# Performance work log

Measured on AMD Instinct MI355X. Metric: run time of the kernel, lower is better.

The kernel has to match this reference:

```python
import jax, jax.numpy as jnp
import numpy as np

POOL = 7                     # cfg.POOLING_SIZE
PRE = 2 * POOL               # pre_pool_size (max_pool=True path)
LEVEL_HW = (256, 128, 64, 32)  # square H=W of P2..P5 for a 1024x1024 image


def setup_inputs() -> dict:
    key = jax.random.key(0)
    ks = jax.random.split(key, 8)
    C = 256
    feats = {f"p{i + 2}": jax.random.normal(ks[i], (1, C, s, s), dtype=jnp.float32)
             for i, s in enumerate(LEVEL_HW)}
    N = 1000
    IMG = 1024.0
    x1 = jax.random.uniform(ks[4], (N,), minval=0.0, maxval=IMG - 33.0)
    y1 = jax.random.uniform(ks[5], (N,), minval=0.0, maxval=IMG - 33.0)
    w = jax.random.uniform(ks[6], (N,), minval=32.0, maxval=512.0)
    h = jax.random.uniform(ks[7], (N,), minval=32.0, maxval=512.0)
    x2 = jnp.minimum(x1 + w, IMG - 1.0)
    y2 = jnp.minimum(y1 + h, IMG - 1.0)
    rois = jnp.stack([jnp.zeros((N,), jnp.float32), x1, y1, x2, y2], axis=1)
    inp = dict(feats)
    inp["rois"] = rois
    return inp


def _crop_pool_fpn(p2, p3, p4, p5, rois):
    """Faithful vectorized version of Network._crop_pool_layer_fpn (max_pool=True).

    Per-ROI FPN level select, affine-grid + bilinear grid_sample
    (align_corners=True semantics, zeros padding), then 2x2 max pool.
    """
    levels = (p2, p3, p4, p5)
    C = p2.shape[1]
    Hm = p2.shape[2]  # largest (P2) map; all levels padded up to this
    # Pad every level into one [L, Hm, Wm, C] array (NHWC for clean gathers).
    feats = jnp.stack([
        jnp.pad(jnp.transpose(f[0], (1, 2, 0)),
                ((0, Hm - f.shape[2]), (0, Hm - f.shape[3]), (0, 0)))
        for f in levels])

    x1, y1, x2, y2 = rois[:, 1], rois[:, 2], rois[:, 3], rois[:, 4]
    w = jnp.where(x2 - x1 <= 0, 1e-14, x2 - x1)
    h = jnp.where(y2 - y1 <= 0, 1e-14, y2 - y1)
    kf = 4.0 + jnp.log2(jnp.sqrt(w * h) / 224.0)   # k0 + log2(sqrt(wh)/224)
    kf = jnp.clip(kf, 2.0, 5.0)                     # clamp BEFORE round (as in source)
    k = jnp.round(kf)
    scale = 2.0 ** k
    lvl = k.astype(jnp.int32) - 2                   # [N] in [0,4)
    x1s, y1s, x2s, y2s = x1 / scale, y1 / scale, x2 / scale, y2 / scale

    # affine_grid(theta) + align_corners=True grid_sample collapses to direct
    # pixel coords: px = (x1+x2)/2 + t*(x2-x1)/2, t = linspace(-1, 1, PRE).
    t = jnp.linspace(-1.0, 1.0, PRE)
    px = (x1s + x2s)[:, None] * 0.5 + t[None, :] * ((x2s - x1s)[:, None] * 0.5)  # [N,PRE]
    py = (y1s + y2s)[:, None] * 0.5 + t[None, :] * ((y2s - y1s)[:, None] * 0.5)
    PX = jnp.broadcast_to(px[:, None, :], (px.shape[0], PRE, PRE))  # [N,PRE,PRE]
    PY = jnp.broadcast_to(py[:, :, None], (py.shape[0], PRE, PRE))

    HWl = jnp.asarray(LEVEL_HW, jnp.float32)[lvl][:, None, None]  # per-ROI level size (square)
    x0 = jnp.floor(PX)
    y0 = jnp.floor(PY)
    dx = PX - x0
    dy = PY - y0

    def gather(yi, xi):
        inb = ((xi >= 0) & (xi < HWl) & (yi >= 0) & (yi < HWl)).astype(feats.dtype)
        yc = jnp.clip(yi, 0, Hm - 1).astype(jnp.int32)
        xc = jnp.clip(xi, 0, Hm - 1).astype(jnp.int32)
        v = feats[lvl[:, None, None], yc, xc]      # [N,PRE,PRE,C]
        return v * inb[..., None]                   # zeros padding

    out = (gather(y0, x0) * ((1 - dy) * (1 - dx))[..., None]
           + gather(y0, x0 + 1) * ((1 - dy) * dx)[..., None]
           + gather(y0 + 1, x0) * (dy * (1 - dx))[..., None]
           + gather(y0 + 1, x0 + 1) * (dy * dx)[..., None])  # [N,PRE,PRE,C]

    crops = jnp.transpose(out, (0, 3, 1, 2))        # [N,C,PRE,PRE]
    N = crops.shape[0]
    crops = crops.reshape(N, C, POOL, 2, POOL, 2).max(axis=(3, 5))  # 2x2 max pool
    return crops                                     # [N,C,POOL,POOL]


def reference(p2, p3, p4, p5, rois):
    return _crop_pool_fpn(p2, p3, p4, p5, rois)
```

## Files before the change

kernel.cpp:

```cpp
#include <hip/hip_runtime.h>
#include <math.h>

#define C_CH 256
#define PRE 14
#define NPOOL 7
#define PIX (NPOOL * NPOOL)
#define OUT_PER_ROI (C_CH * PIX)
#define QTR_OUT (64 * PIX)
#define SROW 68

#define OFF_P2 0
#define OFF_P3 16777216u
#define OFF_P4 20971520u
#define OFF_P5 22020096u
#define WS_ELEMS 22282240u

#define RB 528

static __device__ __forceinline__ unsigned short f2bf(float f) {
    unsigned int u = __float_as_uint(f);
    unsigned int r = (u + 0x7FFFu + ((u >> 16) & 1u)) >> 16;
    return (unsigned short)r;
}
static __device__ __forceinline__ float bfLO(unsigned int u) { return __uint_as_float(u << 16); }
static __device__ __forceinline__ float bfHI(unsigned int u) { return __uint_as_float(u & 0xFFFF0000u); }

static __device__ __forceinline__ float4 bilerp4(uint2 a00, uint2 a01, uint2 a10, uint2 a11, float4 w) {
    float4 r;
    r.x = fmaf(bfLO(a00.x), w.x, fmaf(bfLO(a01.x), w.y, fmaf(bfLO(a10.x), w.z, bfLO(a11.x) * w.w)));
    r.y = fmaf(bfHI(a00.x), w.x, fmaf(bfHI(a01.x), w.y, fmaf(bfHI(a10.x), w.z, bfHI(a11.x) * w.w)));
    r.z = fmaf(bfLO(a00.y), w.x, fmaf(bfLO(a01.y), w.y, fmaf(bfLO(a10.y), w.z, bfLO(a11.y) * w.w)));
    r.w = fmaf(bfHI(a00.y), w.x, fmaf(bfHI(a01.y), w.y, fmaf(bfHI(a10.y), w.z, bfHI(a11.y) * w.w)));
    return r;
}

__global__ __launch_bounds__(256) void transpose_all_k(
    const float* __restrict__ p2, const float* __restrict__ p3,
    const float* __restrict__ p4, const float* __restrict__ p5,
    unsigned short* __restrict__ ws) {
    __shared__ unsigned char lds[128 * RB];

    int b = blockIdx.x;
    const float* __restrict__ src;
    int HW2; unsigned int off;
    if (b < 512)      { src = p2; HW2 = 65536; off = OFF_P2; }
    else if (b < 640) { src = p3; HW2 = 16384; off = OFF_P3; b -= 512; }
    else if (b < 672) { src = p4; HW2 = 4096;  off = OFF_P4; b -= 640; }
    else              { src = p5; HW2 = 1024;  off = OFF_P5; b -= 672; }
    const int hw0 = b << 7;

    const int t   = threadIdx.x;
    const int hwq = t & 31;
    const int cg  = t >> 5;
    const int key = (hwq & 7) << 4;

    #pragma unroll
    for (int s = 0; s < 8; ++s) {
        const int c0 = (cg << 2) + (s << 5);
        const float* g = src + (size_t)c0 * HW2 + hw0 + (hwq << 2);
        const float4 a0 = *(const float4*)(g);
        const float4 a1 = *(const float4*)(g + HW2);
        const float4 a2 = *(const float4*)(g + 2 * (size_t)HW2);
        const float4 a3 = *(const float4*)(g + 3 * (size_t)HW2);
        const int cb = (c0 << 1) ^ key;
        unsigned char* base = &lds[(hwq << 2) * RB + cb];
        ushort4 w;
        w.x = f2bf(a0.x); w.y = f2bf(a1.x); w.z = f2bf(a2.x); w.w = f2bf(a3.x);
        *(ushort4*)(base) = w;
        w.x = f2bf(a0.y); w.y = f2bf(a1.y); w.z = f2bf(a2.y); w.w = f2bf(a3.y);
        *(ushort4*)(base + RB) = w;
        w.x = f2bf(a0.z); w.y = f2bf(a1.z); w.z = f2bf(a2.z); w.w = f2bf(a3.z);
        *(ushort4*)(base + 2 * RB) = w;
        w.x = f2bf(a0.w); w.y = f2bf(a1.w); w.z = f2bf(a2.w); w.w = f2bf(a3.w);
        *(ushort4*)(base + 3 * RB) = w;
    }
    __syncthreads();

    char* __restrict__ dstb = (char*)(ws + off + ((size_t)hw0 << 8));
    const int chunk = t & 31;
    const int hwl   = t >> 5;
    #pragma unroll
    for (int p = 0; p < 16; ++p) {
        const int hw = (p << 3) + hwl;
        const int k2 = ((hw >> 2) & 7) << 4;
        const uint4 v = *(const uint4*)&lds[hw * RB + ((chunk << 4) ^ k2)];
        *(uint4*)(dstb + hw * 512 + (chunk << 4)) = v;
    }
}

template <bool HWC>
__global__ __launch_bounds__(256, 6) void roi_align_k(
    const float* __restrict__ p2, const float* __restrict__ p3,
    const float* __restrict__ p4, const float* __restrict__ p5,
    const unsigned short* __restrict__ ws, const float* __restrict__ rois,
    float* __restrict__ out) {

    __shared__ float sxw0[PRE], sxw1[PRE], syw0[PRE], syw1[PRE];
    __shared__ int   sxc0[PRE], sxc1[PRE], syc0[PRE], syc1[PRE];
    __shared__ float4 wtab[PRE * PRE];
    __shared__ int4   otab[PRE * PRE];
    __shared__ float  sout[PIX * SROW];

    const int n   = blockIdx.x;
    const int ch0 = blockIdx.y << 6;
    const float x1 = rois[n * 5 + 1];
    const float y1 = rois[n * 5 + 2];
    const float x2 = rois[n * 5 + 3];
    const float y2 = rois[n * 5 + 4];

    float w = x2 - x1; w = (w <= 0.f) ? 1e-14f : w;
    float h = y2 - y1; h = (h <= 0.f) ? 1e-14f : h;
    float kf = 4.f + log2f(sqrtf(w * h) * (1.f / 224.f));
    kf = fminf(fmaxf(kf, 2.f), 5.f);
    const float kr = rintf(kf);
    const int   lvl = (int)kr - 2;
    const float scale = exp2f(kr);
    const int   HW = 256 >> lvl;

    const int t = threadIdx.x;

    if (t < 2 * PRE) {
        const bool isx = t < PRE;
        const int  j = isx ? t : t - PRE;
        const float a1 = isx ? x1 : y1;
        const float a2 = isx ? x2 : y2;
        const float a1s = a1 / scale, a2s = a2 / scale;
        const float cen  = (a1s + a2s) * 0.5f;
        const float half = (a2s - a1s) * 0.5f;
        const float tt = -1.f + (2.f / 13.f) * (float)j;
        const float p  = cen + tt * half;
        const float p0 = floorf(p);
        const float d  = p - p0;
        const float HWf = (float)HW;
        const float m0 = (p0 >= 0.f && p0 < HWf) ? 1.f : 0.f;
        const float m1 = (p0 + 1.f >= 0.f && p0 + 1.f < HWf) ? 1.f : 0.f;
        const int c0i = min(max((int)p0, 0), HW - 1);
        const int c1i = min(max((int)p0 + 1, 0), HW - 1);
        if (isx) { sxw0[j] = (1.f - d) * m0; sxw1[j] = d * m1; sxc0[j] = c0i; sxc1[j] = c1i; }
        else     { syw0[j] = (1.f - d) * m0; syw1[j] = d * m1; syc0[j] = c0i; syc1[j] = c1i; }
    }
    __syncthreads();

    if (HWC) {
        for (int s = t; s < PRE * PRE; s += 256) {
            const int i = s / PRE;
            const int j = s - i * PRE;
            wtab[s] = make_float4(syw0[i] * sxw0[j], syw0[i] * sxw1[j],
                                  syw1[i] * sxw0[j], syw1[i] * sxw1[j]);
            otab[s] = make_int4((syc0[i] * HW + sxc0[j]) << 9, (syc0[i] * HW + sxc1[j]) << 9,
                                (syc1[i] * HW + sxc0[j]) << 9, (syc1[i] * HW + sxc1[j]) << 9);
        }
        __syncthreads();
    }

    const int g     = t & 15;
    const int ph    = t >> 4;
    const int cbase = ch0 + (g << 2);

    if (HWC) {
        const unsigned int off = (lvl == 0) ? OFF_P2 : (lvl == 1) ? OFF_P3 : (lvl == 2) ? OFF_P4 : OFF_P5;
        const char* __restrict__ base = (const char*)(ws + off);
        const int cb2 = cbase << 1;

        #define DO_PIXEL(P)                                                           \
        {                                                                             \
            const int p_ = (P);                                                       \
            const int oy_ = p_ / 7;                                                   \
            const int ox_ = p_ - oy_ * 7;                                             \
            const int s00 = oy_ * 28 + (ox_ << 1);                                    \
            const int4  oA = otab[s00];      const float4 wA = wtab[s00];             \
            const int4  oB = otab[s00 + 1];  const float4 wB = wtab[s00 + 1];         \
            const int4  oC = otab[s00 + 14]; const float4 wC = wtab[s00 + 14];        \
            const int4  oD = otab[s00 + 15]; const float4 wD = wtab[s00 + 15];        \
            const uint2 A00 = *(const uint2*)(base + (oA.x + cb2));                   \
            const uint2 A01 = *(const uint2*)(base + (oA.y + cb2));                   \
            const uint2 A10 = *(const uint2*)(base + (oA.z + cb2));                   \
            const uint2 A11 = *(const uint2*)(base + (oA.w + cb2));                   \
            const uint2 B00 = *(const uint2*)(base + (oB.x + cb2));                   \
            const uint2 B01 = *(const uint2*)(base + (oB.y + cb2));                   \
            const uint2 B10 = *(const uint2*)(base + (oB.z + cb2));                   \
            const uint2 B11 = *(const uint2*)(base + (oB.w + cb2));                   \
            const uint2 C00 = *(const uint2*)(base + (oC.x + cb2));                   \
            const uint2 C01 = *(const uint2*)(base + (oC.y + cb2));                   \
            const uint2 C10 = *(const uint2*)(base + (oC.z + cb2));                   \
            const uint2 C11 = *(const uint2*)(base + (oC.w + cb2));                   \
            const uint2 D00 = *(const uint2*)(base + (oD.x + cb2));                   \
            const uint2 D01 = *(const uint2*)(base + (oD.y + cb2));                   \
            const uint2 D10 = *(const uint2*)(base + (oD.z + cb2));                   \
            const uint2 D11 = *(const uint2*)(base + (oD.w + cb2));                   \
            const float4 vA = bilerp4(A00, A01, A10, A11, wA);                        \
            const float4 vB = bilerp4(B00, B01, B10, B11, wB);                        \
            const float4 vC = bilerp4(C00, C01, C10, C11, wC);                        \
            const float4 vD = bilerp4(D00, D01, D10, D11, wD);                        \
            float4 m_;                                                               \
            m_.x = fmaxf(fmaxf(vA.x, vB.x), fmaxf(vC.x, vD.x));                       \
            m_.y = fmaxf(fmaxf(vA.y, vB.y), fmaxf(vC.y, vD.y));                       \
            m_.z = fmaxf(fmaxf(vA.z, vB.z), fmaxf(vC.z, vD.z));                       \
            m_.w = fmaxf(fmaxf(vA.w, vB.w), fmaxf(vC.w, vD.w));                       \
            *(float4*)&sout[p_ * SROW + (g << 2)] = m_;                               \
        }

        DO_PIXEL(ph)
        DO_PIXEL(ph + 16)
        DO_PIXEL(ph + 32)
        if (ph == 0) DO_PIXEL(48)
        #undef DO_PIXEL
    } else {
        const float* __restrict__ fbF = (lvl == 0) ? p2 : (lvl == 1) ? p3 : (lvl == 2) ? p4 : p5;
        const int HW2 = HW * HW;
        for (int p = ph; p < PIX; p += 16) {
            const int oy = p / 7;
            const int ox = p - oy * 7;
            float4 m = make_float4(-3.4e38f, -3.4e38f, -3.4e38f, -3.4e38f);
            #pragma unroll
            for (int sy = 0; sy < 2; ++sy) {
                const int i = oy * 2 + sy;
                const float wy0 = syw0[i], wy1 = syw1[i];
                const int   yc0 = syc0[i], yc1 = syc1[i];
                #pragma unroll
                for (int sx = 0; sx < 2; ++sx) {
                    const int j = ox * 2 + sx;
                    const float w00 = wy0 * sxw0[j], w01 = wy0 * sxw1[j];
                    const float w10 = wy1 * sxw0[j], w11 = wy1 * sxw1[j];
                    const int   xc0 = sxc0[j], xc1 = sxc1[j];
                    float vv[4];
                    #pragma unroll
                    for (int k = 0; k < 4; ++k) {
                        const size_t cb = (size_t)(cbase + k) * HW2;
                        const float a00 = fbF[cb + yc0 * HW + xc0];
                        const float a01 = fbF[cb + yc0 * HW + xc1];
                        const float a10 = fbF[cb + yc1 * HW + xc0];
                        const float a11 = fbF[cb + yc1 * HW + xc1];
                        vv[k] = fmaf(a00, w00, fmaf(a01, w01, fmaf(a10, w10, a11 * w11)));
                    }
                    m.x = fmaxf(m.x, vv[0]);
                    m.y = fmaxf(m.y, vv[1]);
                    m.z = fmaxf(m.z, vv[2]);
                    m.w = fmaxf(m.w, vv[3]);
                }
            }
            *(float4*)&sout[p * SROW + (g << 2)] = m;
        }
    }
    __syncthreads();

    const size_t ob = (size_t)n * OUT_PER_ROI + (size_t)ch0 * PIX;
    for (int o = t; o < QTR_OUT; o += 256) {
        const int c  = o / PIX;
        const int pp = o - c * PIX;
        out[ob + o] = sout[pp * SROW + c];
    }
}

extern "C" void kernel_launch(void* const* d_in, const int* in_sizes, int n_in,
                              void* d_out, int out_size, void* d_ws, size_t ws_size,
                              hipStream_t stream) {
    const float* p2   = (const float*)d_in[0];
    const float* p3   = (const float*)d_in[1];
    const float* p4   = (const float*)d_in[2];
    const float* p5   = (const float*)d_in[3];
    const float* rois = (const float*)d_in[4];
    float* out = (float*)d_out;
    const int N = in_sizes[4] / 5;

    const size_t need = (size_t)WS_ELEMS * sizeof(unsigned short);
    if (ws_size >= need) {
        unsigned short* ws = (unsigned short*)d_ws;
        transpose_all_k<<<680, 256, 0, stream>>>(p2, p3, p4, p5, ws);
        roi_align_k<true><<<dim3(N, 4), 256, 0, stream>>>(p2, p3, p4, p5, ws, rois, out);
    } else {
        roi_align_k<false><<<dim3(N, 4), 256, 0, stream>>>(p2, p3, p4, p5, nullptr, rois, out);
    }
}
```

Baseline: 55.51 us.

## Stage ROI feature window into LDS before bilinear sampling when it fits

New measurement: 67.91 us. 22.3% more time.

```diff
diff --git a/kernel.cpp b/kernel.cpp
--- a/kernel.cpp
+++ b/kernel.cpp
@@ -8,6 +8,7 @@
 #define OUT_PER_ROI (C_CH * PIX)
 #define QTR_OUT (64 * PIX)
 #define SROW 68
+#define WTEX 352
 
 #define OFF_P2 0
 #define OFF_P3 16777216u
@@ -89,7 +90,7 @@
 }
 
 template <bool HWC>
-__global__ __launch_bounds__(256, 6) void roi_align_k(
+__global__ __launch_bounds__(256, 3) void roi_align_k(
     const float* __restrict__ p2, const float* __restrict__ p3,
     const float* __restrict__ p4, const float* __restrict__ p5,
     const unsigned short* __restrict__ ws, const float* __restrict__ rois,
@@ -99,7 +100,7 @@
     __shared__ int   sxc0[PRE], sxc1[PRE], syc0[PRE], syc1[PRE];
     __shared__ float4 wtab[PRE * PRE];
     __shared__ int4   otab[PRE * PRE];
-    __shared__ float  sout[PIX * SROW];
+    __shared__ unsigned char arena[WTEX * 128];
 
     const int n   = blockIdx.x;
     const int ch0 = blockIdx.y << 6;
@@ -141,14 +142,27 @@
     }
     __syncthreads();
 
+    const int xs0 = sxc0[0], xs1 = sxc1[PRE - 1];
+    const int ys0 = syc0[0], ys1 = syc1[PRE - 1];
+    const int wx = xs1 - xs0 + 1;
+    const int wy = ys1 - ys0 + 1;
+    const bool staged = HWC && (wx * wy <= WTEX);
+
     if (HWC) {
         for (int s = t; s < PRE * PRE; s += 256) {
             const int i = s / PRE;
             const int j = s - i * PRE;
             wtab[s] = make_float4(syw0[i] * sxw0[j], syw0[i] * sxw1[j],
                                   syw1[i] * sxw0[j], syw1[i] * sxw1[j]);
-            otab[s] = make_int4((syc0[i] * HW + sxc0[j]) << 9, (syc0[i] * HW + sxc1[j]) << 9,
-                                (syc1[i] * HW + sxc0[j]) << 9, (syc1[i] * HW + sxc1[j]) << 9);
+            if (staged) {
+                const int r0 = (syc0[i] - ys0) * wx - xs0;
+                const int r1 = (syc1[i] - ys0) * wx - xs0;
+                otab[s] = make_int4((r0 + sxc0[j]) << 7, (r0 + sxc1[j]) << 7,
+                                    (r1 + sxc0[j]) << 7, (r1 + sxc1[j]) << 7);
+            } else {
+                otab[s] = make_int4((syc0[i] * HW + sxc0[j]) << 9, (syc0[i] * HW + sxc1[j]) << 9,
+                                    (syc1[i] * HW + sxc0[j]) << 9, (syc1[i] * HW + sxc1[j]) << 9);
+            }
         }
         __syncthreads();
     }
@@ -156,92 +170,132 @@
     const int g     = t & 15;
     const int ph    = t >> 4;
     const int cbase = ch0 + (g << 2);
+    const int g8    = g << 3;
+
+    float4 res0, res1, res2, res3;
 
     if (HWC) {
         const unsigned int off = (lvl == 0) ? OFF_P2 : (lvl == 1) ? OFF_P3 : (lvl == 2) ? OFF_P4 : OFF_P5;
-        const char* __restrict__ base = (const char*)(ws + off);
-        const int cb2 = cbase << 1;
-
-        #define DO_PIXEL(P)                                                           \
+        const char* __restrict__ gws = (const char*)(ws + off);
+
+        if (staged) {
+            const char* __restrict__ gsrc = gws + (ch0 << 1);
+            const int nb = wx * wy << 7;
+            for (int i = t << 4; i < nb; i += 4096) {
+                const int tex = i >> 7;
+                const int within = i & 127;
+                const int r = tex / wx;
+                const int c = tex - r * wx;
+                const uint4 v = *(const uint4*)(gsrc + ((((size_t)(ys0 + r)) * HW + (xs0 + c)) << 9) + within);
+                *(uint4*)&arena[(tex << 7) + (within ^ ((tex & 3) << 5))] = v;
+            }
+            __syncthreads();
+
+            #define LD(o) (*(const uint2*)&arena[(o) + (g8 ^ (((o) >> 2) & 0x60))])
+            #define DO_PIXEL(P, RES)                                                  \
+            {                                                                         \
+                const int p_ = (P);                                                   \
+                const int oy_ = p_ / 7;                                               \
+                const int ox_ = p_ - oy_ * 7;                                         \
+                const int s00 = oy_ * 28 + (ox_ << 1);                                \
+                const int4  oA = otab[s00];      const float4 wA = wtab[s00];         \
+                const int4  oB = otab[s00 + 1];  const float4 wB = wtab[s00 + 1];     \
+                const int4  oC = otab[s00 + 14]; const float4 wC = wtab[s00 + 14];    \
+                const int4  oD = otab[s00 + 15]; const float4 wD = wtab[s00 + 15];    \
+                const float4 vA = bilerp4(LD(oA.x), LD(oA.y), LD(oA.z), LD(oA.w), wA);\
+                const float4 vB = bilerp4(LD(oB.x), LD(oB.y), LD(oB.z), LD(oB.w), wB);\
+                const float4 vC = bilerp4(LD(oC.x), LD(oC.y), LD(oC.z), LD(oC.w), wC);\
+                const float4 vD = bilerp4(LD(oD.x), LD(oD.y), LD(oD.z), LD(oD.w), wD);\
+                RES.x = fmaxf(fmaxf(vA.x, vB.x), fmaxf(vC.x, vD.x));                  \
+                RES.y = fmaxf(fmaxf(vA.y, vB.y), fmaxf(vC.y, vD.y));                  \
+                RES.z = fmaxf(fmaxf(vA.z, vB.z), fmaxf(vC.z, vD.z));                  \
+                RES.w = fmaxf(fmaxf(vA.w, vB.w), fmaxf(vC.w, vD.w));                  \
+            }
+            DO_PIXEL(ph, res0)
+            DO_PIXEL(ph + 16, res1)
+            DO_PIXEL(ph + 32, res2)
+            if (ph == 0) DO_PIXEL(48, res3)
+            #undef DO_PIXEL
+            #undef LD
+        } else {
+            const int cb2 = cbase << 1;
+            #define LD(o) (*(const uint2*)(gws + ((o) + cb2)))
+            #define DO_PIXEL(P, RES)                                                  \
+            {                                                                         \
+                const int p_ = (P);                                                   \
+                const int oy_ = p_ / 7;                                               \
+                const int ox_ = p_ - oy_ * 7;                                         \
+                const int s00 = oy_ * 28 + (ox_ << 1);                                \
+                const int4  oA = otab[s00];      const float4 wA = wtab[s00];         \
+                const int4  oB = otab[s00 + 1];  const float4 wB = wtab[s00 + 1];     \
+                const int4  oC = otab[s00 + 14]; const float4 wC = wtab[s00 + 14];    \
+                const int4  oD = otab[s00 + 15]; const float4 wD = wtab[s00 + 15];    \
+                const uint2 A00 = LD(oA.x), A01 = LD(oA.y), A10 = LD(oA.z), A11 = LD(oA.w); \
+                const uint2 B00 = LD(oB.x), B01 = LD(oB.y), B10 = LD(oB.z), B11 = LD(oB.w); \
+                const uint2 C00 = LD(oC.x), C01 = LD(oC.y), C10 = LD(oC.z), C11 = LD(oC.w); \
+                const uint2 D00 = LD(oD.x), D01 = LD(oD.y), D10 = LD(oD.z), D11 = LD(oD.w); \
+                const float4 vA = bilerp4(A00, A01, A10, A11, wA);                    \
+                const float4 vB = bilerp4(B00, B01, B10, B11, wB);                    \
+                const float4 vC = bilerp4(C00, C01, C10, C11, wC);                    \
+                const float4 vD = bilerp4(D00, D01, D10, D11, wD);                    \
+                RES.x = fmaxf(fmaxf(vA.x, vB.x), fmaxf(vC.x, vD.x));                  \
+                RES.y = fmaxf(fmaxf(vA.y, vB.y), fmaxf(vC.y, vD.y));                  \
+                RES.z = fmaxf(fmaxf(vA.z, vB.z), fmaxf(vC.z, vD.z));                  \
+                RES.w = fmaxf(fmaxf(vA.w, vB.w), fmaxf(vC.w, vD.w));                  \
+            }
+            DO_PIXEL(ph, res0)
+            DO_PIXEL(ph + 16, res1)
+            DO_PIXEL(ph + 32, res2)
+            if (ph == 0) DO_PIXEL(48, res3)
+            #undef DO_PIXEL
+            #undef LD
+        }
+    } else {
+        const float* __restrict__ fbF = (lvl == 0) ? p2 : (lvl == 1) ? p3 : (lvl == 2) ? p4 : p5;
+        const int HW2 = HW * HW;
+        #define DO_PIXEL(P, RES)                                                      \
         {                                                                             \
             const int p_ = (P);                                                       \
             const int oy_ = p_ / 7;                                                   \
             const int ox_ = p_ - oy_ * 7;                                             \
-            const int s00 = oy_ * 28 + (ox_ << 1);                                    \
-            const int4  oA = otab[s00];      const float4 wA = wtab[s00];             \
-            const int4  oB = otab[s00 + 1];  const float4 wB = wtab[s00 + 1];         \
-            const int4  oC = otab[s00 + 14]; const float4 wC = wtab[s00 + 14];        \
-            const int4  oD = otab[s00 + 15]; const float4 wD = wtab[s00 + 15];        \
-            const uint2 A00 = *(const uint2*)(base + (oA.x + cb2));                   \
-            const uint2 A01 = *(const uint2*)(base + (oA.y + cb2));                   \
-            const uint2 A10 = *(const uint2*)(base + (oA.z + cb2));                   \
-            const uint2 A11 = *(const uint2*)(base + (oA.w + cb2));                   \
-            const uint2 B00 = *(const uint2*)(base + (oB.x + cb2));                   \
-            const uint2 B01 = *(const uint2*)(base + (oB.y + cb2));                   \
-            const uint2 B10 = *(const uint2*)(base + (oB.z + cb2));                   \
-            const uint2 B11 = *(const uint2*)(base + (oB.w + cb2));                   \
-            const uint2 C00 = *(const uint2*)(base + (oC.x + cb2));                   \
-            const uint2 C01 = *(const uint2*)(base + (oC.y + cb2));                   \
-            const uint2 C10 = *(const uint2*)(base + (oC.z + cb2));                   \
-            const uint2 C11 = *(const uint2*)(base + (oC.w + cb2));                   \
-            const uint2 D00 = *(const uint2*)(base + (oD.x + cb2));                   \
-            const uint2 D01 = *(const uint2*)(base + (oD.y + cb2));                   \
-            const uint2 D10 = *(const uint2*)(base + (oD.z + cb2));                   \
-            const uint2 D11 = *(const uint2*)(base + (oD.w + cb2));                   \
-            const float4 vA = bilerp4(A00, A01, A10, A11, wA);                        \
-            const float4 vB = bilerp4(B00, B01, B10, B11, wB);                        \
-            const float4 vC = bilerp4(C00, C01, C10, C11, wC);                        \
-            const float4 vD = bilerp4(D00, D01, D10, D11, wD);                        \
-            float4 m_;                                                               \
-            m_.x = fmaxf(fmaxf(vA.x, vB.x), fmaxf(vC.x, vD.x));                       \
-            m_.y = fmaxf(fmaxf(vA.y, vB.y), fmaxf(vC.y, vD.y));                       \
-            m_.z = fmaxf(fmaxf(vA.z, vB.z), fmaxf(vC.z, vD.z));                       \
-            m_.w = fmaxf(fmaxf(vA.w, vB.w), fmaxf(vC.w, vD.w));                       \
-            *(float4*)&sout[p_ * SROW + (g << 2)] = m_;                               \
+            RES = make_float4(-3.4e38f, -3.4e38f, -3.4e38f, -3.4e38f);                \
+            for (int sy = 0; sy < 2; ++sy) {                                          \
+                const int i = oy_ * 2 + sy;                                           \
+                const float wy0 = syw0[i], wy1 = syw1[i];                             \
+                const int   yc0 = syc0[i], yc1 = syc1[i];                             \
+                for (int sx = 0; sx < 2; ++sx) {                                      \
+                    const int j = ox_ * 2 + sx;                                       \
+                    const float w00 = wy0 * sxw0[j], w01 = wy0 * sxw1[j];             \
+                    const float w10 = wy1 * sxw0[j], w11 = wy1 * sxw1[j];             \
+                    const int   xc0 = sxc0[j], xc1 = sxc1[j];                         \
+                    for (int k = 0; k < 4; ++k) {                                     \
+                        const size_t cb = (size_t)(cbase + k) * HW2;                  \
+                        const float a00 = fbF[cb + yc0 * HW + xc0];                   \
+                        const float a01 = fbF[cb + yc0 * HW + xc1];                   \
+                        const float a10 = fbF[cb + yc1 * HW + xc0];                   \
+                        const float a11 = fbF[cb + yc1 * HW + xc1];                   \
+                        const float vv = fmaf(a00, w00, fmaf(a01, w01, fmaf(a10, w10, a11 * w11))); \
+                        if (k == 0) RES.x = fmaxf(RES.x, vv);                         \
+                        else if (k == 1) RES.y = fmaxf(RES.y, vv);                    \
+                        else if (k == 2) RES.z = fmaxf(RES.z, vv);                    \
+                        else RES.w = fmaxf(RES.w, vv);                                \
+                    }                                                                 \
+                }                                                                     \
+            }                                                                         \
         }
-
-        DO_PIXEL(ph)
-        DO_PIXEL(ph + 16)
-        DO_PIXEL(ph + 32)
-        if (ph == 0) DO_PIXEL(48)
+        DO_PIXEL(ph, res0)
+        DO_PIXEL(ph + 16, res1)
+        DO_PIXEL(ph + 32, res2)
+        if (ph == 0) DO_PIXEL(48, res3)
         #undef DO_PIXEL
-    } else {
-        const float* __restrict__ fbF = (lvl == 0) ? p2 : (lvl == 1) ? p3 : (lvl == 2) ? p4 : p5;
-        const int HW2 = HW * HW;
-        for (int p = ph; p < PIX; p += 16) {
-            const int oy = p / 7;
-            const int ox = p - oy * 7;
-            float4 m = make_float4(-3.4e38f, -3.4e38f, -3.4e38f, -3.4e38f);
-            #pragma unroll
-            for (int sy = 0; sy < 2; ++sy) {
-                const int i = oy * 2 + sy;
-                const float wy0 = syw0[i], wy1 = syw1[i];
-                const int   yc0 = syc0[i], yc1 = syc1[i];
-                #pragma unroll
-                for (int sx = 0; sx < 2; ++sx) {
-                    const int j = ox * 2 + sx;
-                    const float w00 = wy0 * sxw0[j], w01 = wy0 * sxw1[j];
-                    const float w10 = wy1 * sxw0[j], w11 = wy1 * sxw1[j];
-                    const int   xc0 = sxc0[j], xc1 = sxc1[j];
-                    float vv[4];
-                    #pragma unroll
-                    for (int k = 0; k < 4; ++k) {
-                        const size_t cb = (size_t)(cbase + k) * HW2;
-                        const float a00 = fbF[cb + yc0 * HW + xc0];
-                        const float a01 = fbF[cb + yc0 * HW + xc1];
-                        const float a10 = fbF[cb + yc1 * HW + xc0];
-                        const float a11 = fbF[cb + yc1 * HW + xc1];
-                        vv[k] = fmaf(a00, w00, fmaf(a01, w01, fmaf(a10, w10, a11 * w11)));
-                    }
-                    m.x = fmaxf(m.x, vv[0]);
-                    m.y = fmaxf(m.y, vv[1]);
-                    m.z = fmaxf(m.z, vv[2]);
-                    m.w = fmaxf(m.w, vv[3]);
-                }
-            }
-            *(float4*)&sout[p * SROW + (g << 2)] = m;
-        }
-    }
+    }
+    __syncthreads();
+
+    float* sout = (float*)arena;
+    *(float4*)&sout[ph * SROW + (g << 2)] = res0;
+    *(float4*)&sout[(ph + 16) * SROW + (g << 2)] = res1;
+    *(float4*)&sout[(ph + 32) * SROW + (g << 2)] = res2;
+    if (ph == 0) *(float4*)&sout[48 * SROW + (g << 2)] = res3;
     __syncthreads();
 
     const size_t ob = (size_t)n * OUT_PER_ROI + (size_t)ch0 * PIX;
```
